# Performance work log

Measured on AMD Instinct MI355X. Metric: run time of the kernel, lower is better.

The kernel has to match this reference:

```python
import jax, jax.numpy as jnp
import numpy as np

BETA = 0.5

def setup_inputs() -> dict:
    key = jax.random.key(0)
    ks = jax.random.split(key, 10)
    B, H = 4096, 200
    ITEM, REGION = 100000, 1000
    D, HID = 128, 64  # embed_size, hidden_size
    half = D // 2
    history = jax.random.randint(ks[0], (B, H), 0, ITEM)
    target = jax.random.randint(ks[1], (B,), 0, ITEM)
    history_region = jax.random.randint(ks[2], (B, H), 0, REGION)
    target_region = jax.random.randint(ks[3], (B,), 0, REGION)
    W_hist = jax.random.normal(ks[4], (ITEM, half), jnp.float32) * 0.01
    W_tgt = jax.random.normal(ks[5], (ITEM, half), jnp.float32) * 0.01
    W_reg = jax.random.normal(ks[6], (REGION, half), jnp.float32) * 0.01
    W1 = jax.random.normal(ks[7], (D, HID), jnp.float32) * (1.0 / np.sqrt(D))
    b1 = jnp.zeros((HID,), jnp.float32)
    W2 = jax.random.normal(ks[8], (HID,), jnp.float32) * (1.0 / np.sqrt(HID))
    return {"history": history, "target": target,
            "history_region": history_region, "target_region": target_region,
            "W_hist": W_hist, "W_tgt": W_tgt, "W_reg": W_reg,
            "W1": W1, "b1": b1, "W2": W2}

def reference(history, target, history_region, target_region,
              W_hist, W_tgt, W_reg, W1, b1, W2):
    # gather + concat: [B,H,D] and [B,D]
    h = jnp.concatenate([W_hist[history], W_reg[history_region]], axis=-1)
    t = jnp.concatenate([W_tgt[target], W_reg[target_region]], axis=-1)
    inp = h * t[:, None, :]                      # [B,H,D]
    r1 = jax.nn.relu(inp @ W1 + b1)              # [B,H,HID] (dropout = identity at eval)
    logits = r1 @ W2                             # [B,H]
    mask = (history != target[:, None]).astype(logits.dtype)
    exp_A = jnp.exp(logits) * mask               # [B,H]
    exp_sum = jnp.sum(exp_A, axis=-1) ** BETA    # [B], beta-power normalization
    attn = exp_A / exp_sum[:, None]              # [B,H]
    pred = jnp.einsum('bhd,bd->b', h * attn[..., None], t)
    return jax.nn.sigmoid(pred)
```

## Files before the change

### kernel.cpp

```cpp
#include <hip/hip_runtime.h>
#include <math.h>

#define NB        4096
#define NH        200
#define HIST_ROWS 100000
#define REG_ROWS  1000
#define NTILES    13

typedef __attribute__((ext_vector_type(4))) int   int4i;

#define SA 2048.0f
#define SB 16384.0f
#define ST 2048.0f
#define INV_LOGIT (1.0f / (SA * SB))
#define INV_S     (1.0f / (SA * ST))

__device__ __forceinline__ int q8(float x, float s) {
    return __float2int_rn(fminf(fmaxf(x * s, -127.f), 127.f));
}
__device__ __forceinline__ int pack4(float a, float b, float c, float d, float s) {
    const int x0 = q8(a, s), x1 = q8(b, s), x2 = q8(c, s), x3 = q8(d, s);
    return (x0 & 255) | ((x1 & 255) << 8) | ((x2 & 255) << 16) | (x3 << 24);
}

__global__ __launch_bounds__(256) void prep_i8(
    const float* __restrict__ Wh, const float* __restrict__ Wr,
    const float* __restrict__ W1,
    unsigned char* __restrict__ tab, float* __restrict__ W1F2)
{
    const int total = (HIST_ROWS + REG_ROWS) * 16;
    const int HE    = HIST_ROWS * 16;
    unsigned* dst = (unsigned*)tab;
    for (int i = blockIdx.x * blockDim.x + threadIdx.x; i < total;
         i += gridDim.x * blockDim.x) {
        const float4 v = (i < HE) ? ((const float4*)Wh)[i]
                                  : ((const float4*)Wr)[i - HE];
        dst[i] = (unsigned)pack4(v.x, v.y, v.z, v.w, SA);
    }
    if (blockIdx.x == 0) {
        for (int i = threadIdx.x; i < 10240; i += 256) {
            const int chunk = i >> 4, j = i & 15;
            const int frag = chunk >> 6, nt = frag >> 1, ks = frag & 1;
            const int c = chunk & 63, q = c >> 4, l = c & 15;
            W1F2[i] = (nt < 4) ? W1[(ks * 64 + q * 16 + j) * 64 + nt * 16 + l] : 0.f;
        }
    }
}

__device__ __forceinline__ void epi_store_i8(
    const int4i* accT, const float* w2v, const float* b1v,
    int tl, int quad, int l15, float* logit_lds, float* s_lds)
{
    float part[4] = {0.f, 0.f, 0.f, 0.f};
    #pragma unroll
    for (int nt = 0; nt < 4; ++nt)
        #pragma unroll
        for (int r = 0; r < 4; ++r)
            part[r] += fmaxf((float)accT[nt][r] * INV_LOGIT + b1v[nt], 0.f) * w2v[nt];
    #pragma unroll
    for (int r = 0; r < 4; ++r) {
        part[r] += __shfl_xor(part[r], 1);
        part[r] += __shfl_xor(part[r], 2);
        part[r] += __shfl_xor(part[r], 4);
        part[r] += __shfl_xor(part[r], 8);
    }
    if (l15 == 0) {
        const int jg = tl * 16 + quad * 4;
        #pragma unroll
        for (int r = 0; r < 4; ++r) {
            logit_lds[jg + r] = part[r];
            s_lds[jg + r]     = (float)accT[4][r] * INV_S;
        }
    }
}

__device__ __forceinline__ int4i quant_row_fp32(const float* row, int quad) {
    const float4* p = (const float4*)(row + quad * 16);
    const float4 v0 = p[0], v1 = p[1], v2 = p[2], v3 = p[3];
    int4i o;
    o.x = pack4(v0.x, v0.y, v0.z, v0.w, SA);
    o.y = pack4(v1.x, v1.y, v1.z, v1.w, SA);
    o.z = pack4(v2.x, v2.y, v2.z, v2.w, SA);
    o.w = pack4(v3.x, v3.y, v3.z, v3.w, SA);
    return o;
}

template <bool BT>
__global__ __launch_bounds__(256, 3) void nais_i8(
    const int*   __restrict__ history,
    const int*   __restrict__ target,
    const int*   __restrict__ history_region,
    const int*   __restrict__ target_region,
    const float* __restrict__ W_hist,
    const float* __restrict__ W_tgt,
    const float* __restrict__ W_reg,
    const float* __restrict__ W1,
    const float* __restrict__ b1,
    const float* __restrict__ W2,
    const unsigned char* __restrict__ tab,
    const float* __restrict__ W1F2,
    float*       __restrict__ out)
{
    __shared__ int hist_lds[224];
    __shared__ int hreg_lds[224];
    __shared__ __align__(16) float t_lds[128];
    __shared__ __align__(16) int Bf4[640 * 4];
    __shared__ float logit_lds[208];
    __shared__ float s_lds[208];
    __shared__ float red_e[4], red_p[4];

    const int b   = blockIdx.x;
    const int tid = threadIdx.x;
    const int tgt = target[b];

    if (tid < 224) {
        const int jj = tid < NH ? tid : NH - 1;
        hist_lds[tid] = history[b * NH + jj];
        hreg_lds[tid] = history_region[b * NH + jj];
    }
    if (tid < 64) {
        t_lds[tid] = W_tgt[(size_t)tgt * 64 + tid];
    } else if (tid < 128) {
        t_lds[tid] = W_reg[(size_t)target_region[b] * 64 + (tid - 64)];
    }
    __syncthreads();

    const int lane = tid & 63, wv = tid >> 6;
    const int l15  = lane & 15, quad = lane >> 4;

    const int  tls[4] = {wv, wv + 4, wv + 8, wv + 12};
    const bool has3   = (tls[3] < NTILES);

    int4i A[4][2];
    if (BT) {
        #pragma unroll
        for (int tt = 0; tt < 4; ++tt) {
            const int j  = ((tt == 3 && !has3) ? tls[2] : tls[tt]) * 16 + l15;
            const int ih = hist_lds[j], ir = hreg_lds[j];
            A[tt][0] = *(const int4i*)(tab + (size_t)ih * 64 + quad * 16);
            A[tt][1] = *(const int4i*)(tab + (size_t)(HIST_ROWS + ir) * 64 + quad * 16);
        }
    }

    #pragma unroll
    for (int v = 0; v < 3; ++v) {
        const int i = tid + v * 256;
        if (i < 640) {
            const int frag = i >> 6, nt = frag >> 1, ks = frag & 1;
            const int c = i & 63, q = c >> 4, l = c & 15;
            const int k0 = ks * 64 + q * 16;
            const float4 t0 = *(const float4*)(t_lds + k0);
            const float4 t1 = *(const float4*)(t_lds + k0 + 4);
            const float4 t2 = *(const float4*)(t_lds + k0 + 8);
            const float4 t3 = *(const float4*)(t_lds + k0 + 12);
            int4i ob;
            if (nt < 4) {
                float4 w0, w1, w2, w3;
                if (BT) {
                    const float4* wp = (const float4*)(W1F2 + i * 16);
                    w0 = wp[0]; w1 = wp[1]; w2 = wp[2]; w3 = wp[3];
                } else {
                    const int n = nt * 16 + l;
                    float tmp[16];
                    #pragma unroll
                    for (int j = 0; j < 16; ++j) tmp[j] = W1[(k0 + j) * 64 + n];
                    w0 = make_float4(tmp[0], tmp[1], tmp[2], tmp[3]);
                    w1 = make_float4(tmp[4], tmp[5], tmp[6], tmp[7]);
                    w2 = make_float4(tmp[8], tmp[9], tmp[10], tmp[11]);
                    w3 = make_float4(tmp[12], tmp[13], tmp[14], tmp[15]);
                }
                ob.x = pack4(w0.x * t0.x, w0.y * t0.y, w0.z * t0.z, w0.w * t0.w, SB);
                ob.y = pack4(w1.x * t1.x, w1.y * t1.y, w1.z * t1.z, w1.w * t1.w, SB);
                ob.z = pack4(w2.x * t2.x, w2.y * t2.y, w2.z * t2.z, w2.w * t2.w, SB);
                ob.w = pack4(w3.x * t3.x, w3.y * t3.y, w3.z * t3.z, w3.w * t3.w, SB);
            } else {
                if (l == 0) {
                    ob.x = pack4(t0.x, t0.y, t0.z, t0.w, ST);
                    ob.y = pack4(t1.x, t1.y, t1.z, t1.w, ST);
                    ob.z = pack4(t2.x, t2.y, t2.z, t2.w, ST);
                    ob.w = pack4(t3.x, t3.y, t3.z, t3.w, ST);
                } else {
                    ob = (int4i){0, 0, 0, 0};
                }
            }
            *reinterpret_cast<int4i*>(&Bf4[i * 4]) = ob;
        }
    }
    __syncthreads();

    float w2v[4], b1v[4];
    #pragma unroll
    for (int nt = 0; nt < 4; ++nt) {
        w2v[nt] = W2[nt * 16 + l15];
        b1v[nt] = b1[nt * 16 + l15];
    }

    #pragma unroll
    for (int pp = 0; pp < 2; ++pp) {
        const int t0i = pp * 2, t1i = pp * 2 + 1;
        const bool hb = (t1i < 3) || has3;

        if (!BT) {
            #pragma unroll
            for (int tt = 0; tt < 2; ++tt) {
                const int ti = t0i + tt;
                const int j  = ((ti == 3 && !has3) ? tls[2] : tls[ti]) * 16 + l15;
                A[ti][0] = quant_row_fp32(W_hist + (size_t)hist_lds[j] * 64, quad);
                A[ti][1] = quant_row_fp32(W_reg  + (size_t)hreg_lds[j] * 64, quad);
            }
        }

        int4i acc[2][5];
        #pragma unroll
        for (int tt = 0; tt < 2; ++tt)
            #pragma unroll
            for (int nt = 0; nt < 5; ++nt) acc[tt][nt] = (int4i){0, 0, 0, 0};

        #pragma unroll
        for (int ks = 0; ks < 2; ++ks) {
            int4i bf[5];
            #pragma unroll
            for (int nt = 0; nt < 5; ++nt)
                bf[nt] = *reinterpret_cast<const int4i*>(&Bf4[((nt * 2 + ks) * 64 + lane) * 4]);
            #pragma unroll
            for (int nt = 0; nt < 5; ++nt)
                acc[0][nt] = __builtin_amdgcn_mfma_i32_16x16x64_i8(A[t0i][ks], bf[nt], acc[0][nt], 0, 0, 0);
            if (hb) {
                #pragma unroll
                for (int nt = 0; nt < 5; ++nt)
                    acc[1][nt] = __builtin_amdgcn_mfma_i32_16x16x64_i8(A[t1i][ks], bf[nt], acc[1][nt], 0, 0, 0);
            }
        }

        epi_store_i8(acc[0], w2v, b1v, tls[t0i], quad, l15, logit_lds, s_lds);
        if (hb) epi_store_i8(acc[1], w2v, b1v, tls[t1i], quad, l15, logit_lds, s_lds);
    }
    __syncthreads();

    float e = 0.f, p = 0.f;
    if (tid < NH) {
        const float ex = (hist_lds[tid] != tgt) ? expf(logit_lds[tid]) : 0.f;
        e = ex;
        p = ex * s_lds[tid];
    }
    #pragma unroll
    for (int off = 32; off > 0; off >>= 1) {
        e += __shfl_down(e, off);
        p += __shfl_down(p, off);
    }
    if (lane == 0) { red_e[wv] = e; red_p[wv] = p; }
    __syncthreads();
    if (tid == 0) {
        const float E = red_e[0] + red_e[1] + red_e[2] + red_e[3];
        const float P = red_p[0] + red_p[1] + red_p[2] + red_p[3];
        const float pred = P / sqrtf(E);
        out[b] = 1.f / (1.f + expf(-pred));
    }
}

extern "C" void kernel_launch(void* const* d_in, const int* in_sizes, int n_in,
                              void* d_out, int out_size, void* d_ws, size_t ws_size,
                              hipStream_t stream) {
    const int*   history        = (const int*)  d_in[0];
    const int*   target         = (const int*)  d_in[1];
    const int*   history_region = (const int*)  d_in[2];
    const int*   target_region  = (const int*)  d_in[3];
    const float* W_hist         = (const float*)d_in[4];
    const float* W_tgt          = (const float*)d_in[5];
    const float* W_reg          = (const float*)d_in[6];
    const float* W1             = (const float*)d_in[7];
    const float* b1             = (const float*)d_in[8];
    const float* W2             = (const float*)d_in[9];
    float* out = (float*)d_out;

    const size_t tab_bytes = (size_t)(HIST_ROWS + REG_ROWS) * 64;
    const size_t need = tab_bytes + 10240 * 4;
    if (ws_size >= need) {
        unsigned char* tab = (unsigned char*)d_ws;
        float* W1F2 = (float*)((char*)d_ws + tab_bytes);
        prep_i8<<<2048, 256, 0, stream>>>(W_hist, W_reg, W1, tab, W1F2);
        nais_i8<true><<<NB, 256, 0, stream>>>(history, target, history_region, target_region,
                                              W_hist, W_tgt, W_reg, W1, b1, W2, tab, W1F2, out);
    } else {
        nais_i8<false><<<NB, 256, 0, stream>>>(history, target, history_region, target_region,
                                               W_hist, W_tgt, W_reg, W1, b1, W2, nullptr, nullptr, out);
    }
}
```

Before: 145.4 us.

## Process one batch row per wavefront with register-resident B fragments and prefetch ring

Replaces the one-block-per-row int8 MFMA kernel with a kernel where each wavefront handles a full batch row. B fragments are built directly in registers from W1F2 and the target embeddings, and all 13 tiles are iterated with a 5-slot prefetch ring of gathered int8 rows. The softmax reduction uses shuffles instead of LDS and block barriers. The W1F2 reorder in prep is spread across the grid rather than done only in block 0. Register pressure rises, and B fragments are rebuilt per wavefront rather than shared through LDS.

```diff
diff --git a/kernel.cpp b/kernel.cpp
--- a/kernel.cpp
+++ b/kernel.cpp
@@ -28,6 +28,13 @@
     const float* __restrict__ W1,
     unsigned char* __restrict__ tab, float* __restrict__ W1F2)
 {
+    for (int i = blockIdx.x * blockDim.x + threadIdx.x; i < 10240;
+         i += gridDim.x * blockDim.x) {
+        const int chunk = i >> 4, j = i & 15;
+        const int frag = chunk >> 6, nt = frag >> 1, ks = frag & 1;
+        const int c = chunk & 63, q = c >> 4, l = c & 15;
+        W1F2[i] = (nt < 4) ? W1[(ks * 64 + q * 16 + j) * 64 + nt * 16 + l] : 0.f;
+    }
     const int total = (HIST_ROWS + REG_ROWS) * 16;
     const int HE    = HIST_ROWS * 16;
     unsigned* dst = (unsigned*)tab;
@@ -37,13 +44,140 @@
                                   : ((const float4*)Wr)[i - HE];
         dst[i] = (unsigned)pack4(v.x, v.y, v.z, v.w, SA);
     }
-    if (blockIdx.x == 0) {
-        for (int i = threadIdx.x; i < 10240; i += 256) {
-            const int chunk = i >> 4, j = i & 15;
-            const int frag = chunk >> 6, nt = frag >> 1, ks = frag & 1;
-            const int c = chunk & 63, q = c >> 4, l = c & 15;
-            W1F2[i] = (nt < 4) ? W1[(ks * 64 + q * 16 + j) * 64 + nt * 16 + l] : 0.f;
-        }
+}
+
+__global__ __launch_bounds__(256, 3) void nais_wv(
+    const int*   __restrict__ history,
+    const int*   __restrict__ target,
+    const int*   __restrict__ history_region,
+    const int*   __restrict__ target_region,
+    const float* __restrict__ W_tgt,
+    const float* __restrict__ W_reg,
+    const float* __restrict__ b1,
+    const float* __restrict__ W2,
+    const unsigned char* __restrict__ tab,
+    const float* __restrict__ W1F2,
+    float*       __restrict__ out)
+{
+    const int tid  = threadIdx.x;
+    const int lane = tid & 63, wv = tid >> 6;
+    const int b    = blockIdx.x * 4 + wv;
+    const int l15  = lane & 15, quad = lane >> 4;
+
+    const int tgt  = target[b];
+    const int treg = target_region[b];
+
+    int ih[NTILES], ir[NTILES];
+    #pragma unroll
+    for (int t = 0; t < NTILES; ++t) {
+        int j = t * 16 + l15;
+        if (j >= NH) j = NH - 1;
+        ih[t] = history[b * NH + j];
+        ir[t] = history_region[b * NH + j];
+    }
+
+    int4i Ab[5][2];
+    #pragma unroll
+    for (int t = 0; t < 4; ++t) {
+        Ab[t][0] = *(const int4i*)(tab + (size_t)ih[t] * 64 + quad * 16);
+        Ab[t][1] = *(const int4i*)(tab + (size_t)(HIST_ROWS + ir[t]) * 64 + quad * 16);
+    }
+
+    const float* tW = W_tgt + (size_t)tgt * 64;
+    const float* rW = W_reg + (size_t)treg * 64;
+    int4i bf[10];
+    #pragma unroll
+    for (int v = 0; v < 10; ++v) {
+        const int nt = v >> 1, ks = v & 1;
+        const float4* tp = (const float4*)(((ks == 0) ? tW : rW) + quad * 16);
+        const float4 t0 = tp[0], t1 = tp[1], t2 = tp[2], t3 = tp[3];
+        int4i ob;
+        if (nt < 4) {
+            const float4* wp = (const float4*)(W1F2 + (v * 64 + lane) * 16);
+            const float4 w0 = wp[0], w1 = wp[1], w2 = wp[2], w3 = wp[3];
+            ob.x = pack4(w0.x * t0.x, w0.y * t0.y, w0.z * t0.z, w0.w * t0.w, SB);
+            ob.y = pack4(w1.x * t1.x, w1.y * t1.y, w1.z * t1.z, w1.w * t1.w, SB);
+            ob.z = pack4(w2.x * t2.x, w2.y * t2.y, w2.z * t2.z, w2.w * t2.w, SB);
+            ob.w = pack4(w3.x * t3.x, w3.y * t3.y, w3.z * t3.z, w3.w * t3.w, SB);
+        } else {
+            if (l15 == 0) {
+                ob.x = pack4(t0.x, t0.y, t0.z, t0.w, ST);
+                ob.y = pack4(t1.x, t1.y, t1.z, t1.w, ST);
+                ob.z = pack4(t2.x, t2.y, t2.z, t2.w, ST);
+                ob.w = pack4(t3.x, t3.y, t3.z, t3.w, ST);
+            } else {
+                ob = (int4i){0, 0, 0, 0};
+            }
+        }
+        bf[v] = ob;
+    }
+
+    float w2v[4], b1v[4];
+    #pragma unroll
+    for (int nt = 0; nt < 4; ++nt) {
+        w2v[nt] = W2[nt * 16 + l15];
+        b1v[nt] = b1[nt * 16 + l15];
+    }
+
+    float e_acc = 0.f, p_acc = 0.f;
+    const int r_sel = l15 & 3;
+
+    #pragma unroll
+    for (int t = 0; t < NTILES; ++t) {
+        if (t + 4 < NTILES) {
+            const int s = (t + 4) % 5;
+            Ab[s][0] = *(const int4i*)(tab + (size_t)ih[t + 4] * 64 + quad * 16);
+            Ab[s][1] = *(const int4i*)(tab + (size_t)(HIST_ROWS + ir[t + 4]) * 64 + quad * 16);
+        }
+        const int sl = t % 5;
+
+        int4i acc[5];
+        #pragma unroll
+        for (int nt = 0; nt < 5; ++nt) acc[nt] = (int4i){0, 0, 0, 0};
+        #pragma unroll
+        for (int ks = 0; ks < 2; ++ks)
+            #pragma unroll
+            for (int nt = 0; nt < 5; ++nt)
+                acc[nt] = __builtin_amdgcn_mfma_i32_16x16x64_i8(Ab[sl][ks], bf[nt * 2 + ks], acc[nt], 0, 0, 0);
+
+        float part[4] = {0.f, 0.f, 0.f, 0.f};
+        #pragma unroll
+        for (int nt = 0; nt < 4; ++nt)
+            #pragma unroll
+            for (int r = 0; r < 4; ++r)
+                part[r] += fmaxf((float)acc[nt][r] * INV_LOGIT + b1v[nt], 0.f) * w2v[nt];
+        #pragma unroll
+        for (int r = 0; r < 4; ++r) {
+            part[r] += __shfl_xor(part[r], 1);
+            part[r] += __shfl_xor(part[r], 2);
+            part[r] += __shfl_xor(part[r], 4);
+            part[r] += __shfl_xor(part[r], 8);
+        }
+        const float lgA = (r_sel & 1) ? part[1] : part[0];
+        const float lgB = (r_sel & 1) ? part[3] : part[2];
+        const float lg  = (r_sel & 2) ? lgB : lgA;
+        float sv[4];
+        #pragma unroll
+        for (int r = 0; r < 4; ++r) sv[r] = (float)__shfl(acc[4][r], lane & 48);
+        const float svA = (r_sel & 1) ? sv[1] : sv[0];
+        const float svB = (r_sel & 1) ? sv[3] : sv[2];
+        const float s_own = ((r_sel & 2) ? svB : svA) * INV_S;
+        const int  ihj  = __shfl(ih[t], quad * 4 + r_sel);
+        const int  jrow = t * 16 + quad * 4 + r_sel;
+        const bool valid = (l15 < 4) && (jrow < NH) && (ihj != tgt);
+        const float ex = valid ? expf(lg) : 0.f;
+        e_acc += ex;
+        p_acc += ex * s_own;
+    }
+
+    #pragma unroll
+    for (int off = 1; off < 64; off <<= 1) {
+        e_acc += __shfl_xor(e_acc, off);
+        p_acc += __shfl_xor(p_acc, off);
+    }
+    if (lane == 0) {
+        const float pred = p_acc / sqrtf(e_acc);
+        out[b] = 1.f / (1.f + expf(-pred));
     }
 }
 
@@ -85,8 +219,7 @@
     return o;
 }
 
-template <bool BT>
-__global__ __launch_bounds__(256, 3) void nais_i8(
+__global__ __launch_bounds__(256, 3) void nais_fb(
     const int*   __restrict__ history,
     const int*   __restrict__ target,
     const int*   __restrict__ history_region,
@@ -97,8 +230,6 @@
     const float* __restrict__ W1,
     const float* __restrict__ b1,
     const float* __restrict__ W2,
-    const unsigned char* __restrict__ tab,
-    const float* __restrict__ W1F2,
     float*       __restrict__ out)
 {
     __shared__ int hist_lds[224];
@@ -127,20 +258,8 @@
 
     const int lane = tid & 63, wv = tid >> 6;
     const int l15  = lane & 15, quad = lane >> 4;
-
     const int  tls[4] = {wv, wv + 4, wv + 8, wv + 12};
     const bool has3   = (tls[3] < NTILES);
-
-    int4i A[4][2];
-    if (BT) {
-        #pragma unroll
-        for (int tt = 0; tt < 4; ++tt) {
-            const int j  = ((tt == 3 && !has3) ? tls[2] : tls[tt]) * 16 + l15;
-            const int ih = hist_lds[j], ir = hreg_lds[j];
-            A[tt][0] = *(const int4i*)(tab + (size_t)ih * 64 + quad * 16);
-            A[tt][1] = *(const int4i*)(tab + (size_t)(HIST_ROWS + ir) * 64 + quad * 16);
-        }
-    }
 
     #pragma unroll
     for (int v = 0; v < 3; ++v) {
@@ -155,24 +274,14 @@
             const float4 t3 = *(const float4*)(t_lds + k0 + 12);
             int4i ob;
             if (nt < 4) {
-                float4 w0, w1, w2, w3;
-                if (BT) {
-                    const float4* wp = (const float4*)(W1F2 + i * 16);
-                    w0 = wp[0]; w1 = wp[1]; w2 = wp[2]; w3 = wp[3];
-                } else {
-                    const int n = nt * 16 + l;
-                    float tmp[16];
-                    #pragma unroll
-                    for (int j = 0; j < 16; ++j) tmp[j] = W1[(k0 + j) * 64 + n];
-                    w0 = make_float4(tmp[0], tmp[1], tmp[2], tmp[3]);
-                    w1 = make_float4(tmp[4], tmp[5], tmp[6], tmp[7]);
-                    w2 = make_float4(tmp[8], tmp[9], tmp[10], tmp[11]);
-                    w3 = make_float4(tmp[12], tmp[13], tmp[14], tmp[15]);
-                }
-                ob.x = pack4(w0.x * t0.x, w0.y * t0.y, w0.z * t0.z, w0.w * t0.w, SB);
-                ob.y = pack4(w1.x * t1.x, w1.y * t1.y, w1.z * t1.z, w1.w * t1.w, SB);
-                ob.z = pack4(w2.x * t2.x, w2.y * t2.y, w2.z * t2.z, w2.w * t2.w, SB);
-                ob.w = pack4(w3.x * t3.x, w3.y * t3.y, w3.z * t3.z, w3.w * t3.w, SB);
+                const int n = nt * 16 + l;
+                float tmp[16];
+                #pragma unroll
+                for (int j = 0; j < 16; ++j) tmp[j] = W1[(k0 + j) * 64 + n];
+                ob.x = pack4(tmp[0] * t0.x, tmp[1] * t0.y, tmp[2] * t0.z, tmp[3] * t0.w, SB);
+                ob.y = pack4(tmp[4] * t1.x, tmp[5] * t1.y, tmp[6] * t1.z, tmp[7] * t1.w, SB);
+                ob.z = pack4(tmp[8] * t2.x, tmp[9] * t2.y, tmp[10] * t2.z, tmp[11] * t2.w, SB);
+                ob.w = pack4(tmp[12] * t3.x, tmp[13] * t3.y, tmp[14] * t3.z, tmp[15] * t3.w, SB);
             } else {
                 if (l == 0) {
                     ob.x = pack4(t0.x, t0.y, t0.z, t0.w, ST);
@@ -195,19 +304,18 @@
         b1v[nt] = b1[nt * 16 + l15];
     }
 
+    int4i A[4][2];
     #pragma unroll
     for (int pp = 0; pp < 2; ++pp) {
         const int t0i = pp * 2, t1i = pp * 2 + 1;
         const bool hb = (t1i < 3) || has3;
 
-        if (!BT) {
-            #pragma unroll
-            for (int tt = 0; tt < 2; ++tt) {
-                const int ti = t0i + tt;
-                const int j  = ((ti == 3 && !has3) ? tls[2] : tls[ti]) * 16 + l15;
-                A[ti][0] = quant_row_fp32(W_hist + (size_t)hist_lds[j] * 64, quad);
-                A[ti][1] = quant_row_fp32(W_reg  + (size_t)hreg_lds[j] * 64, quad);
-            }
+        #pragma unroll
+        for (int tt = 0; tt < 2; ++tt) {
+            const int ti = t0i + tt;
+            const int j  = ((ti == 3 && !has3) ? tls[2] : tls[ti]) * 16 + l15;
+            A[ti][0] = quant_row_fp32(W_hist + (size_t)hist_lds[j] * 64, quad);
+            A[ti][1] = quant_row_fp32(W_reg  + (size_t)hreg_lds[j] * 64, quad);
         }
 
         int4i acc[2][5];
@@ -218,17 +326,17 @@
 
         #pragma unroll
         for (int ks = 0; ks < 2; ++ks) {
-            int4i bf[5];
+            int4i bfr[5];
             #pragma unroll
             for (int nt = 0; nt < 5; ++nt)
-                bf[nt] = *reinterpret_cast<const int4i*>(&Bf4[((nt * 2 + ks) * 64 + lane) * 4]);
+                bfr[nt] = *reinterpret_cast<const int4i*>(&Bf4[((nt * 2 + ks) * 64 + lane) * 4]);
             #pragma unroll
             for (int nt = 0; nt < 5; ++nt)
-                acc[0][nt] = __builtin_amdgcn_mfma_i32_16x16x64_i8(A[t0i][ks], bf[nt], acc[0][nt], 0, 0, 0);
+                acc[0][nt] = __builtin_amdgcn_mfma_i32_16x16x64_i8(A[t0i][ks], bfr[nt], acc[0][nt], 0, 0, 0);
             if (hb) {
                 #pragma unroll
                 for (int nt = 0; nt < 5; ++nt)
-                    acc[1][nt] = __builtin_amdgcn_mfma_i32_16x16x64_i8(A[t1i][ks], bf[nt], acc[1][nt], 0, 0, 0);
+                    acc[1][nt] = __builtin_amdgcn_mfma_i32_16x16x64_i8(A[t1i][ks], bfr[nt], acc[1][nt], 0, 0, 0);
             }
         }
 
@@ -279,10 +387,10 @@
         unsigned char* tab = (unsigned char*)d_ws;
         float* W1F2 = (float*)((char*)d_ws + tab_bytes);
         prep_i8<<<2048, 256, 0, stream>>>(W_hist, W_reg, W1, tab, W1F2);
-        nais_i8<true><<<NB, 256, 0, stream>>>(history, target, history_region, target_region,
-                                              W_hist, W_tgt, W_reg, W1, b1, W2, tab, W1F2, out);
+        nais_wv<<<NB / 4, 256, 0, stream>>>(history, target, history_region, target_region,
+                                            W_tgt, W_reg, b1, W2, tab, W1F2, out);
     } else {
-        nais_i8<false><<<NB, 256, 0, stream>>>(history, target, history_region, target_region,
-                                               W_hist, W_tgt, W_reg, W1, b1, W2, nullptr, nullptr, out);
-    }
-}
+        nais_fb<<<NB, 256, 0, stream>>>(history, target, history_region, target_region,
+                                        W_hist, W_tgt, W_reg, W1, b1, W2, out);
+    }
+}
```

Result: slower. 181.3 us (+24.7%).
